# Kernel optimization log

Hardware: AMD Instinct MI355X
Metric: run time of the kernel (lower is better)

The kernel has to match this reference:

```python
import jax, jax.numpy as jnp
import numpy as np

N = 50000
NUM_GRAPHS = 64
EPS = 1e-16  # PyG softmax denominator epsilon


def _gat_conv(x, src, dst, W, a_src, a_dst, b, heads, out_ch):
    n = x.shape[0]
    h = (x @ W).reshape(n, heads, out_ch)                    # [N,H,C]
    al_s = jnp.einsum('nhc,hc->nh', h, a_src)                # [N,H]
    al_d = jnp.einsum('nhc,hc->nh', h, a_dst)                # [N,H]
    e = jax.nn.leaky_relu(al_s[src] + al_d[dst], 0.2)        # [E,H]
    emax = jax.ops.segment_max(e, dst, num_segments=n)       # [N,H]
    ee = jnp.exp(e - emax[dst])
    den = jax.ops.segment_sum(ee, dst, num_segments=n)       # [N,H]
    alpha = ee / (den[dst] + EPS)                            # [E,H]
    msg = h[src] * alpha[:, :, None]                         # [E,H,C]
    out = jax.ops.segment_sum(msg, dst, num_segments=n)      # [N,H,C]
    return out.reshape(n, heads * out_ch) + b


def setup_inputs() -> dict:
    key = jax.random.key(0)
    ks = jax.random.split(key, 16)
    E = 250000
    x = jax.random.normal(ks[0], (N, 11), dtype=jnp.float32)
    edge_index = jax.random.randint(ks[1], (2, E), 0, N, dtype=jnp.int64)
    batch = jnp.sort(jax.random.randint(ks[2], (N,), 0, NUM_GRAPHS, dtype=jnp.int64))
    def glorot(k, shape):
        fan = shape[0] + shape[-1]
        return jax.random.uniform(k, shape, jnp.float32, -1.0, 1.0) * np.sqrt(6.0 / fan)
    return {
        'x': x, 'edge_index': edge_index, 'batch': batch,
        'W1': glorot(ks[3], (11, 8 * 128)),
        'a1s': glorot(ks[4], (8, 128)), 'a1d': glorot(ks[5], (8, 128)),
        'b1': jnp.zeros((8 * 128,), jnp.float32),
        'W2': glorot(ks[6], (1024, 8 * 64)),
        'a2s': glorot(ks[7], (8, 64)), 'a2d': glorot(ks[8], (8, 64)),
        'b2': jnp.zeros((8 * 64,), jnp.float32),
        'W3': glorot(ks[9], (512, 4 * 32)),
        'a3s': glorot(ks[10], (4, 32)), 'a3d': glorot(ks[11], (4, 32)),
        'b3': jnp.zeros((4 * 32,), jnp.float32),
        'Wout': glorot(ks[12], (128, 1)),
        'bout': jnp.zeros((1,), jnp.float32),
    }


def reference(x, edge_index, batch, W1, a1s, a1d, b1, W2, a2s, a2d, b2,
              W3, a3s, a3d, b3, Wout, bout):
    n = x.shape[0]
    # GATConv adds self-loops by default
    loop = jnp.arange(n, dtype=edge_index.dtype)
    src = jnp.concatenate([edge_index[0], loop])
    dst = jnp.concatenate([edge_index[1], loop])
    h = jax.nn.leaky_relu(_gat_conv(x, src, dst, W1, a1s, a1d, b1, 8, 128), 0.01)
    h = jax.nn.leaky_relu(_gat_conv(h, src, dst, W2, a2s, a2d, b2, 8, 64), 0.01)
    h = jax.nn.leaky_relu(_gat_conv(h, src, dst, W3, a3s, a3d, b3, 4, 32), 0.01)
    # global mean pool over graphs
    sums = jax.ops.segment_sum(h, batch, num_segments=NUM_GRAPHS)      # [G,128]
    cnt = jax.ops.segment_sum(jnp.ones((n,), h.dtype), batch, num_segments=NUM_GRAPHS)
    pooled = sums / jnp.maximum(cnt, 1.0)[:, None]
    return pooled @ Wout + bout                                        # [G,1]
```

## Files before the change

kernel.cpp:

```cpp
#include <hip/hip_runtime.h>

#define EPS 1e-16f

typedef __attribute__((ext_vector_type(8))) short short8;
typedef __attribute__((ext_vector_type(4))) float f32x4;

__device__ __forceinline__ float b2f(unsigned short u) {
    return __uint_as_float(((unsigned)u) << 16);
}
__device__ __forceinline__ unsigned short f2b(float f) {
    unsigned u = __float_as_uint(f);
    u += 0x7fffu + ((u >> 16) & 1u);
    return (unsigned short)(u >> 16);
}

typedef __attribute__((address_space(3))) void lds_vp;
typedef __attribute__((address_space(1))) const void glb_vp;
__device__ __forceinline__ void load_lds16(const unsigned short* g,
                                           unsigned short* l) {
    __builtin_amdgcn_global_load_lds((glb_vp*)g, (lds_vp*)l, 16, 0, 0);
}

__global__ void init_deg_kernel(int* deg, int N) {
    int i = blockIdx.x * blockDim.x + threadIdx.x;
    if (i < N) deg[i] = 1;
}

__global__ void hist_kernel(const int* __restrict__ ei, int E, int N, int* deg) {
    int e = blockIdx.x * blockDim.x + threadIdx.x;
    if (e < E) {
        int d = ei[E + e];
        if ((unsigned)d < (unsigned)N) atomicAdd(&deg[d], 1);
    }
}

__global__ void scan_block_kernel(const int* __restrict__ deg,
                                  int* __restrict__ rowst,
                                  int* __restrict__ bsum, int N) {
    __shared__ int s[256];
    int t = threadIdx.x, b = blockIdx.x;
    int i = b * 256 + t;
    s[t] = (i < N) ? deg[i] : 0;
    __syncthreads();
    for (int o = 1; o < 256; o <<= 1) {
        int a = (t >= o) ? s[t - o] : 0;
        __syncthreads();
        s[t] += a;
        __syncthreads();
    }
    if (i < N) rowst[i + 1] = s[t];
    if (t == 255) bsum[b] = s[255];
}

__global__ void scan_top_kernel(const int* __restrict__ bsum,
                                int* __restrict__ boff, int NB) {
    __shared__ int psum[65];
    int t = threadIdx.x;
    int chunk = (NB + 63) / 64;
    int lo = t * chunk, hi = lo + chunk;
    if (lo > NB) lo = NB;
    if (hi > NB) hi = NB;
    int s = 0;
    for (int i = lo; i < hi; i++) s += bsum[i];
    psum[t + 1] = s;
    __syncthreads();
    if (t == 0) {
        psum[0] = 0;
        for (int i = 1; i <= 64; i++) psum[i] += psum[i - 1];
    }
    __syncthreads();
    int run = psum[t];
    for (int i = lo; i < hi; i++) {
        boff[i] = run;
        run += bsum[i];
    }
}

__global__ void scan_finish_kernel(int* __restrict__ rowst,
                                   const int* __restrict__ boff,
                                   const int* __restrict__ deg,
                                   int* __restrict__ srcs,
                                   int* __restrict__ cursor, int N) {
    int i = blockIdx.x * 256 + threadIdx.x;
    if (i == 0) rowst[0] = 0;
    if (i < N) {
        int incl = rowst[i + 1] + boff[blockIdx.x];
        rowst[i + 1] = incl;
        int st = incl - deg[i];
        srcs[st] = i;
        cursor[i] = st + 1;
    }
}

__global__ void scatter_kernel(const int* __restrict__ ei, int E, int N,
                               int* cursor, int* srcs) {
    int e = blockIdx.x * blockDim.x + threadIdx.x;
    if (e < E) {
        int d = ei[E + e];
        if ((unsigned)d < (unsigned)N) {
            int p = atomicAdd(&cursor[d], 1);
            int s = ei[e];
            if ((unsigned)s >= (unsigned)N) s = d;
            srcs[p] = s;
        }
    }
}

__global__ void wprep_kernel(const float* __restrict__ W1,
                             const float* __restrict__ W2,
                             const float* __restrict__ W3,
                             unsigned short* __restrict__ wt2,
                             unsigned short* __restrict__ wt3,
                             unsigned short* __restrict__ w1sk) {
    int i = blockIdx.x * blockDim.x + threadIdx.x;
    if (i < 1024 * 512) {
        int k = i / 512, n = i % 512;
        wt2[(size_t)n * 1024 + k] = f2b(W2[i]);
    } else if (i < 1024 * 512 + 512 * 128) {
        int j = i - 1024 * 512;
        int k = j / 128, n = j % 128;
        wt3[(size_t)n * 512 + k] = f2b(W3[j]);
    } else if (i < 1024 * 512 + 512 * 128 + 8 * 128 * 32) {
        int q = i - (1024 * 512 + 512 * 128);
        int h = q >> 12, rem = q & 4095;
        int c = rem >> 5, kk = rem & 31;
        int off = (h == 7) ? 16 : 0;
        float v = 0.f;
        int k = kk - off;
        if (k >= 0 && k < 11) v = W1[k * 1024 + h * 128 + c];
        w1sk[q] = f2b(v);
    }
}

__global__ void wa1_kernel(const float* __restrict__ W1,
                           const float* __restrict__ a1s,
                           const float* __restrict__ a1d,
                           float* __restrict__ w_as, float* __restrict__ w_ad) {
    int t = threadIdx.x;
    if (t >= 88) return;
    int h = t / 11, k = t % 11;
    float s = 0.f, d = 0.f;
    for (int c = 0; c < 128; c++) {
        float w = W1[k * 1024 + h * 128 + c];
        s += w * a1s[h * 128 + c];
        d += w * a1d[h * 128 + c];
    }
    w_as[h * 16 + k] = s;
    w_ad[h * 16 + k] = d;
}

__global__ void al1_kernel(const float* __restrict__ x,
                           const float* __restrict__ w_as,
                           const float* __restrict__ w_ad,
                           float* __restrict__ als, float* __restrict__ ald,
                           int N) {
    int i = blockIdx.x * blockDim.x + threadIdx.x;
    if (i >= N * 8) return;
    int n = i >> 3, h = i & 7;
    float s = 0.f, d = 0.f;
#pragma unroll
    for (int k = 0; k < 11; k++) {
        float xv = x[n * 11 + k];
        s += xv * w_as[h * 16 + k];
        d += xv * w_ad[h * 16 + k];
    }
    als[i] = s;
    ald[i] = d;
}

template <int H>
__global__ void mden_kernel(const float* __restrict__ als,
                            const float* __restrict__ ald,
                            const int* __restrict__ rowst,
                            const int* __restrict__ srcs,
                            float* __restrict__ escr, int N) {
    int i = blockIdx.x * blockDim.x + threadIdx.x;
    if (i >= N * H) return;
    int n = i / H, h = i % H;
    float aldn = ald[i];
    int start = rowst[n], end = rowst[n + 1];
    const int CH = 4;
    float m = -1e30f;
    for (int idx = start; idx < end; idx += CH) {
        int mc = end - idx;
        if (mc > CH) mc = CH;
        int ss[CH];
        float lv[CH];
#pragma unroll
        for (int j = 0; j < CH; j++)
            if (j < mc) ss[j] = srcs[idx + j];
#pragma unroll
        for (int j = 0; j < CH; j++)
            if (j < mc) lv[j] = als[ss[j] * H + h];
#pragma unroll
        for (int j = 0; j < CH; j++)
            if (j < mc) {
                float v = lv[j] + aldn;
                v = v > 0.f ? v : 0.2f * v;
                escr[(size_t)(idx + j) * H + h] = v;
                m = fmaxf(m, v);
            }
    }
    float den = 0.f;
    for (int idx = start; idx < end; idx += CH) {
        int mc = end - idx;
        if (mc > CH) mc = CH;
        float lv[CH];
#pragma unroll
        for (int j = 0; j < CH; j++)
            if (j < mc) lv[j] = escr[(size_t)(idx + j) * H + h];
#pragma unroll
        for (int j = 0; j < CH; j++)
            if (j < mc) den += expf(lv[j] - m);
    }
    float dinv = 1.0f / (den + EPS);
    for (int idx = start; idx < end; idx += CH) {
        int mc = end - idx;
        if (mc > CH) mc = CH;
        float lv[CH];
#pragma unroll
        for (int j = 0; j < CH; j++)
            if (j < mc) lv[j] = escr[(size_t)(idx + j) * H + h];
#pragma unroll
        for (int j = 0; j < CH; j++)
            if (j < mc)
                escr[(size_t)(idx + j) * H + h] = expf(lv[j] - m) * dinv;
    }
}

__global__ void aggx_kernel(const float* __restrict__ x,
                            const float* __restrict__ escr,
                            const int* __restrict__ rowst,
                            const int* __restrict__ srcs,
                            unsigned short* __restrict__ A2, int N) {
    int n = blockIdx.x;
    int t = threadIdx.x;
    int h = t >> 4, k = t & 15;
    int start = rowst[n], end = rowst[n + 1];
    float acc = 0.f;
    const int CH = 4;
    for (int idx = start; idx < end; idx += CH) {
        int mc = end - idx;
        if (mc > CH) mc = CH;
        int ss[CH];
        float av[CH], xv[CH];
#pragma unroll
        for (int j = 0; j < CH; j++)
            if (j < mc) ss[j] = srcs[idx + j];
#pragma unroll
        for (int j = 0; j < CH; j++)
            if (j < mc) av[j] = escr[(size_t)(idx + j) * 8 + h];
#pragma unroll
        for (int j = 0; j < CH; j++)
            if (j < mc) xv[j] = (k < 11) ? x[ss[j] * 11 + k] : 0.f;
#pragma unroll
        for (int j = 0; j < CH; j++)
            if (j < mc) acc += av[j] * xv[j];
    }
    A2[(size_t)n * 128 + t] = f2b(acc);
}

template <bool EPI, int HB, int CC, bool SK>
__global__ __launch_bounds__(256) void gemm_mfma(
    const unsigned short* __restrict__ A, const unsigned short* __restrict__ Bt,
    unsigned short* __restrict__ C, const float* __restrict__ bias,
    const float* __restrict__ a_s, const float* __restrict__ a_d,
    float* __restrict__ als, float* __restrict__ ald, int H, int M, int N,
    int K, int lda) {
    int NX = gridDim.x;
    int bid = blockIdx.y * NX + blockIdx.x;
    int win = bid & (8 * NX - 1);
    int mg = bid / (8 * NX);
    int m_t = mg * 8 + (win & 7);
    int n_t = win >> 3;
    int bm = m_t * 128, bn = n_t * 128;
    if (bm >= M) return;

    union SMem {
        struct {
            unsigned short As[2][128 * 32];
            unsigned short Bs[2][128 * 32];
        } k;
        unsigned short Ct[128 * 132];
    };
    __shared__ __align__(16) SMem sm;
    auto& As = sm.k.As;
    auto& Bs = sm.k.Bs;
    auto& Ct = sm.Ct;

    int t = threadIdx.x;
    int w = t >> 6, lane = t & 63;
    int quad = lane >> 4, l16 = lane & 15;
    int wr = (w >> 1) * 64, wc = (w & 1) * 64;

    int kofs = 0;
    const unsigned short* Bb = Bt;
    if (SK) {
        kofs = n_t * 16;
        if (kofs > lda - 32) kofs = lda - 32;
        Bb = Bt + (size_t)n_t * 128 * 32;
    }

    int c0 = w * 128 + lane;
    int c1 = c0 + 64;
    int r0 = c0 >> 2, p0 = c0 & 3;
    int r1 = c1 >> 2, p1 = c1 & 3;
    int j0 = (p0 - (r0 >> 1)) & 3;
    int j1 = (p1 - (r1 >> 1)) & 3;
    int ga0 = bm + r0;
    if (ga0 >= M) ga0 = M - 1;
    int ga1 = bm + r1;
    if (ga1 >= M) ga1 = M - 1;
    const unsigned short* Ag0 = A + (size_t)ga0 * lda + kofs + j0 * 8;
    const unsigned short* Ag1 = A + (size_t)ga1 * lda + kofs + j1 * 8;
    size_t br0 = SK ? (size_t)r0 : (size_t)(bn + r0);
    size_t br1 = SK ? (size_t)r1 : (size_t)(bn + r1);
    const unsigned short* Bg0 = Bb + br0 * K + j0 * 8;
    const unsigned short* Bg1 = Bb + br1 * K + j1 * 8;

    auto stage = [&](int st, int k0) {
        load_lds16(Ag0 + k0, &As[st][(w * 128) * 8]);
        load_lds16(Ag1 + k0, &As[st][(w * 128 + 64) * 8]);
        load_lds16(Bg0 + k0, &Bs[st][(w * 128) * 8]);
        load_lds16(Bg1 + k0, &Bs[st][(w * 128 + 64) * 8]);
    };

    int aoff[4], boff4[4];
#pragma unroll
    for (int i = 0; i < 4; i++) {
        int ra = wr + i * 16 + l16;
        aoff[i] = ra * 32 + (((quad + (ra >> 1)) & 3) * 8);
        int rb = wc + i * 16 + l16;
        boff4[i] = rb * 32 + (((quad + (rb >> 1)) & 3) * 8);
    }

    f32x4 acc[4][4] = {};
    stage(0, 0);
    int st = 0;
    for (int k0 = 0; k0 < K; k0 += 32, st ^= 1) {
        __syncthreads();
        if (k0 + 32 < K) stage(st ^ 1, k0 + 32);
        short8 a[4], b[4];
#pragma unroll
        for (int mi = 0; mi < 4; mi++) a[mi] = *(const short8*)&As[st][aoff[mi]];
#pragma unroll
        for (int ni = 0; ni < 4; ni++) b[ni] = *(const short8*)&Bs[st][boff4[ni]];
#pragma unroll
        for (int mi = 0; mi < 4; mi++)
#pragma unroll
            for (int ni = 0; ni < 4; ni++)
                acc[mi][ni] = __builtin_amdgcn_mfma_f32_16x16x32_bf16(
                    a[mi], b[ni], acc[mi][ni], 0, 0, 0);
    }
    __syncthreads();

#pragma unroll
    for (int mi = 0; mi < 4; mi++) {
#pragma unroll
        for (int r = 0; r < 4; r++) {
            int rl = wr + mi * 16 + quad * 4 + r;
#pragma unroll
            for (int ni = 0; ni < 4; ni++) {
                int cl = wc + ni * 16 + l16;
                float v = acc[mi][ni][r];
                if (EPI) {
                    v += bias[bn + cl];
                    v = v > 0.f ? v : 0.01f * v;
                }
                Ct[rl * 132 + cl] = f2b(v);
            }
        }
    }
    __syncthreads();
#pragma unroll
    for (int p = 0; p < 16; p++) {
        int q = p * 256 + t;
        int row = q >> 5, c8 = q & 31;
        if (bm + row < M) {
            uint2 v = *(const uint2*)&Ct[row * 132 + c8 * 4];
            *(uint2*)&C[(size_t)(bm + row) * N + bn + c8 * 4] = v;
        }
    }
    if (HB > 0) {
        for (int pi = t; pi < 128 * HB; pi += 256) {
            int row = pi / HB, hl = pi % HB;
            if (bm + row >= M) continue;
            int hg = bn / CC + hl;
            const unsigned short* rp = &Ct[row * 132 + hl * CC];
            const float* asp = a_s + hg * CC;
            const float* adp = a_d + hg * CC;
            float s = 0.f, d = 0.f;
#pragma unroll
            for (int c = 0; c < CC; c++) {
                float v = b2f(rp[c]);
                s += v * asp[c];
                d += v * adp[c];
            }
            als[(size_t)(bm + row) * H + hg] = s;
            ald[(size_t)(bm + row) * H + hg] = d;
        }
    }
}

template <int H, int C>
__global__ void agg_fused4(const unsigned short* __restrict__ hin,
                           const float* __restrict__ als,
                           const float* __restrict__ ald,
                           const int* __restrict__ rowst,
                           const int* __restrict__ srcs,
                           const float* __restrict__ bias,
                           unsigned short* __restrict__ out, int N) {
    constexpr int HC = H * C;
    constexpr int TPH = C / 4;
    int n = blockIdx.x;
    int t = threadIdx.x;
    int c = t * 4;
    int hh = c / C;
    int li = (c % C) / 4;
    int start = rowst[n], end = rowst[n + 1];
    float aldn = ald[n * H + hh];
    float m = -1e30f;
    for (int idx = start + li; idx < end; idx += TPH) {
        float v = als[srcs[idx] * H + hh] + aldn;
        v = v > 0.f ? v : 0.2f * v;
        m = fmaxf(m, v);
    }
#pragma unroll
    for (int o = 1; o < TPH; o <<= 1) m = fmaxf(m, __shfl_xor(m, o));
    float den = 0.f;
    for (int idx = start + li; idx < end; idx += TPH) {
        float v = als[srcs[idx] * H + hh] + aldn;
        v = v > 0.f ? v : 0.2f * v;
        den += expf(v - m);
    }
#pragma unroll
    for (int o = 1; o < TPH; o <<= 1) den += __shfl_xor(den, o);
    float dinv = 1.0f / (den + EPS);

    float a0 = 0.f, a1 = 0.f, a2 = 0.f, a3 = 0.f;
    const int CH = 4;
    for (int idx = start; idx < end; idx += CH) {
        int mc = end - idx;
        if (mc > CH) mc = CH;
        int ss[CH];
        float lv[CH];
        ushort4 uv[CH];
#pragma unroll
        for (int j = 0; j < CH; j++)
            if (j < mc) ss[j] = srcs[idx + j];
#pragma unroll
        for (int j = 0; j < CH; j++)
            if (j < mc) lv[j] = als[ss[j] * H + hh];
#pragma unroll
        for (int j = 0; j < CH; j++)
            if (j < mc) uv[j] = *(const ushort4*)(hin + (size_t)ss[j] * HC + c);
#pragma unroll
        for (int j = 0; j < CH; j++)
            if (j < mc) {
                float v = lv[j] + aldn;
                v = v > 0.f ? v : 0.2f * v;
                float a = expf(v - m) * dinv;
                a0 += a * b2f(uv[j].x);
                a1 += a * b2f(uv[j].y);
                a2 += a * b2f(uv[j].z);
                a3 += a * b2f(uv[j].w);
            }
    }
    float v0 = a0 + bias[c], v1 = a1 + bias[c + 1];
    float v2 = a2 + bias[c + 2], v3 = a3 + bias[c + 3];
    ushort4 o;
    o.x = f2b(v0 > 0.f ? v0 : 0.01f * v0);
    o.y = f2b(v1 > 0.f ? v1 : 0.01f * v1);
    o.z = f2b(v2 > 0.f ? v2 : 0.01f * v2);
    o.w = f2b(v3 > 0.f ? v3 : 0.01f * v3);
    *(ushort4*)&out[(size_t)n * HC + c] = o;
}

template <int H, int C>
__global__ void agg_fused2(const unsigned short* __restrict__ hin,
                           const float* __restrict__ als,
                           const float* __restrict__ ald,
                           const int* __restrict__ rowst,
                           const int* __restrict__ srcs,
                           const float* __restrict__ bias,
                           unsigned short* __restrict__ out, int N) {
    constexpr int HC = H * C;
    constexpr int TPH = C / 2;
    int n = blockIdx.x;
    int t = threadIdx.x;
    int c = t * 2;
    int hh = c / C;
    int li = (c % C) / 2;
    int start = rowst[n], end = rowst[n + 1];
    float aldn = ald[n * H + hh];
    float m = -1e30f;
    for (int idx = start + li; idx < end; idx += TPH) {
        float v = als[srcs[idx] * H + hh] + aldn;
        v = v > 0.f ? v : 0.2f * v;
        m = fmaxf(m, v);
    }
#pragma unroll
    for (int o = 1; o < TPH; o <<= 1) m = fmaxf(m, __shfl_xor(m, o));
    float den = 0.f;
    for (int idx = start + li; idx < end; idx += TPH) {
        float v = als[srcs[idx] * H + hh] + aldn;
        v = v > 0.f ? v : 0.2f * v;
        den += expf(v - m);
    }
#pragma unroll
    for (int o = 1; o < TPH; o <<= 1) den += __shfl_xor(den, o);
    float dinv = 1.0f / (den + EPS);

    float a0 = 0.f, a1 = 0.f;
    const int CH = 4;
    for (int idx = start; idx < end; idx += CH) {
        int mc = end - idx;
        if (mc > CH) mc = CH;
        int ss[CH];
        float lv[CH];
        ushort2 uv[CH];
#pragma unroll
        for (int j = 0; j < CH; j++)
            if (j < mc) ss[j] = srcs[idx + j];
#pragma unroll
        for (int j = 0; j < CH; j++)
            if (j < mc) lv[j] = als[ss[j] * H + hh];
#pragma unroll
        for (int j = 0; j < CH; j++)
            if (j < mc) uv[j] = *(const ushort2*)(hin + (size_t)ss[j] * HC + c);
#pragma unroll
        for (int j = 0; j < CH; j++)
            if (j < mc) {
                float v = lv[j] + aldn;
                v = v > 0.f ? v : 0.2f * v;
                float a = expf(v - m) * dinv;
                a0 += a * b2f(uv[j].x);
                a1 += a * b2f(uv[j].y);
            }
    }
    float v0 = a0 + bias[c], v1 = a1 + bias[c + 1];
    ushort2 o;
    o.x = f2b(v0 > 0.f ? v0 : 0.01f * v0);
    o.y = f2b(v1 > 0.f ? v1 : 0.01f * v1);
    *(ushort2*)&out[(size_t)n * HC + c] = o;
}

__global__ void pool_init_kernel(float* pool, int GC) {
    int i = blockIdx.x * blockDim.x + threadIdx.x;
    if (i < GC) pool[i] = 0.f;
}

__global__ void pool_partial_kernel(const unsigned short* __restrict__ h3,
                                    const int* __restrict__ batch,
                                    float* __restrict__ pool, int N, int G) {
    int lo = blockIdx.x * 128;
    int hi = lo + 128;
    if (hi > N) hi = N;
    if (lo >= N) return;
    int t = threadIdx.x;
    int cur = batch[lo];
    float acc = 0.f;
    for (int n = lo; n < hi; n++) {
        int g = batch[n];
        if (g != cur) {
            if ((unsigned)cur < (unsigned)G) atomicAdd(&pool[cur * 128 + t], acc);
            acc = 0.f;
            cur = g;
        }
        acc += b2f(h3[(size_t)n * 128 + t]);
    }
    if ((unsigned)cur < (unsigned)G) atomicAdd(&pool[cur * 128 + t], acc);
}

__global__ void head_kernel(const float* __restrict__ pool,
                            const int* __restrict__ batch,
                            const float* __restrict__ Wout,
                            const float* __restrict__ bout,
                            float* __restrict__ out, int N) {
    int g = blockIdx.x;
    int t = threadIdx.x;
    int lo, hi;
    {
        int a = 0, b = N;
        while (a < b) { int mid = (a + b) >> 1; if (batch[mid] < g) a = mid + 1; else b = mid; }
        lo = a;
        a = lo; b = N;
        while (a < b) { int mid = (a + b) >> 1; if (batch[mid] < g + 1) a = mid + 1; else b = mid; }
        hi = a;
    }
    float c = (float)(hi - lo);
    c = c > 1.f ? c : 1.f;
    float v = (pool[g * 128 + t] / c) * Wout[t];
    for (int o = 32; o; o >>= 1) v += __shfl_xor(v, o);
    __shared__ float partial[2];
    if ((t & 63) == 0) partial[t >> 6] = v;
    __syncthreads();
    if (t == 0) out[g] = partial[0] + partial[1] + bout[0];
}

extern "C" void kernel_launch(void* const* d_in, const int* in_sizes, int n_in,
                              void* d_out, int out_size, void* d_ws,
                              size_t ws_size, hipStream_t stream) {
    const float* x = (const float*)d_in[0];
    const int* ei = (const int*)d_in[1];
    const int* batch = (const int*)d_in[2];
    const float* W1 = (const float*)d_in[3];
    const float* a1s = (const float*)d_in[4];
    const float* a1d = (const float*)d_in[5];
    const float* b1 = (const float*)d_in[6];
    const float* W2 = (const float*)d_in[7];
    const float* a2s = (const float*)d_in[8];
    const float* a2d = (const float*)d_in[9];
    const float* b2 = (const float*)d_in[10];
    const float* W3 = (const float*)d_in[11];
    const float* a3s = (const float*)d_in[12];
    const float* a3d = (const float*)d_in[13];
    const float* b3 = (const float*)d_in[14];
    const float* Wout = (const float*)d_in[15];
    const float* bout = (const float*)d_in[16];
    float* out = (float*)d_out;

    const int N = in_sizes[0] / 11;
    const int E = in_sizes[1] / 2;
    const int Etot = E + N;
    const int G = out_size;
    const int NB = (N + 255) / 256;
    const int MT = ((N + 127) / 128 + 7) / 8 * 8;

    char* ws = (char*)d_ws;
    size_t off = 0;
    auto alloc = [&](size_t bytes) -> void* {
        void* p = ws + off;
        off += (bytes + 255) & ~(size_t)255;
        return p;
    };
    unsigned short* buf1 = (unsigned short*)alloc((size_t)N * 1024 * 2);
    unsigned short* buf2 = (unsigned short*)alloc((size_t)N * 1024 * 2);
    float* als = (float*)alloc((size_t)N * 8 * 4);
    float* ald = (float*)alloc((size_t)N * 8 * 4);
    float* escr = (float*)alloc((size_t)Etot * 8 * 4);
    int* rowst = (int*)alloc((size_t)(N + 1) * 4);
    int* cursor = (int*)alloc((size_t)N * 4);
    int* srcs = (int*)alloc((size_t)Etot * 4);
    int* deg = (int*)alloc((size_t)N * 4);
    int* bsum = (int*)alloc((size_t)NB * 4);
    int* boff = (int*)alloc((size_t)NB * 4);
    float* pool = (float*)alloc((size_t)G * 128 * 4);
    unsigned short* aggx = (unsigned short*)alloc((size_t)N * 128 * 2);
    unsigned short* w1sk = (unsigned short*)alloc((size_t)8 * 128 * 32 * 2);
    unsigned short* wt2 = (unsigned short*)alloc((size_t)1024 * 512 * 2);
    unsigned short* wt3 = (unsigned short*)alloc((size_t)512 * 128 * 2);
    float* w_as = (float*)alloc(8 * 16 * 4);
    float* w_ad = (float*)alloc(8 * 16 * 4);

    int nb = (N + 255) / 256;
    int eb = (E + 255) / 256;

    init_deg_kernel<<<nb, 256, 0, stream>>>(deg, N);
    hist_kernel<<<eb, 256, 0, stream>>>(ei, E, N, deg);
    scan_block_kernel<<<NB, 256, 0, stream>>>(deg, rowst, bsum, N);
    scan_top_kernel<<<1, 64, 0, stream>>>(bsum, boff, NB);
    scan_finish_kernel<<<NB, 256, 0, stream>>>(rowst, boff, deg, srcs, cursor,
                                               N);
    scatter_kernel<<<eb, 256, 0, stream>>>(ei, E, N, cursor, srcs);

    const int WTOT = 1024 * 512 + 512 * 128 + 8 * 128 * 32;
    wprep_kernel<<<(WTOT + 255) / 256, 256, 0, stream>>>(W1, W2, W3, wt2, wt3,
                                                         w1sk);
    wa1_kernel<<<1, 128, 0, stream>>>(W1, a1s, a1d, w_as, w_ad);

    al1_kernel<<<(N * 8 + 255) / 256, 256, 0, stream>>>(x, w_as, w_ad, als, ald,
                                                        N);
    mden_kernel<8><<<(N * 8 + 255) / 256, 256, 0, stream>>>(als, ald, rowst,
                                                            srcs, escr, N);
    aggx_kernel<<<N, 128, 0, stream>>>(x, escr, rowst, srcs, aggx, N);
    gemm_mfma<true, 0, 1, true><<<dim3(8, MT), 256, 0, stream>>>(
        aggx, w1sk, buf2, b1, nullptr, nullptr, nullptr, nullptr, 0, N, 1024,
        32, 128);

    gemm_mfma<false, 2, 64, false><<<dim3(4, MT), 256, 0, stream>>>(
        buf2, wt2, buf1, nullptr, a2s, a2d, als, ald, 8, N, 512, 1024, 1024);
    agg_fused4<8, 64><<<N, 128, 0, stream>>>(buf1, als, ald, rowst, srcs, b2,
                                             buf2, N);

    gemm_mfma<false, 4, 32, false><<<dim3(1, MT), 256, 0, stream>>>(
        buf2, wt3, buf1, nullptr, a3s, a3d, als, ald, 4, N, 128, 512, 512);
    agg_fused2<4, 32><<<N, 64, 0, stream>>>(buf1, als, ald, rowst, srcs, b3,
                                            buf2, N);

    pool_init_kernel<<<(G * 128 + 255) / 256, 256, 0, stream>>>(pool, G * 128);
    pool_partial_kernel<<<(N + 127) / 128, 128, 0, stream>>>(buf2, batch, pool,
                                                             N, G);
    head_kernel<<<G, 128, 0, stream>>>(pool, batch, Wout, bout, out, N);
}
```

Measured before the change: 482.3 us.

## Add double-buffered async-LDS MFMA GEMM with swizzle and tile raster for layers 2-3

Adds a new gemm_pipe kernel that stages A and B tiles into LDS through global_load_lds with a two-deep buffer, so the next K-tile loads while MFMAs run on the current one. It uses an XOR-swizzled LDS layout, groups blocks into 8-row M windows for L2 reuse, and shares LDS between the staging buffers and the output tile through a union. Layers 2 and 3 now call it in place of gemm_mfma. In exchange it adds hand-placed waitcnt and barriers that depend on exact vmcnt accounting, and uses more LDS per block.

```diff
diff --git a/kernel.cpp b/kernel.cpp
--- a/kernel.cpp
+++ b/kernel.cpp
@@ -387,6 +387,144 @@
             if (bm + row >= M) continue;
             int hg = bn / CC + hl;
             const unsigned short* rp = &Ct[row * 132 + hl * CC];
+            const float* asp = a_s + hg * CC;
+            const float* adp = a_d + hg * CC;
+            float s = 0.f, d = 0.f;
+#pragma unroll
+            for (int c = 0; c < CC; c++) {
+                float v = b2f(rp[c]);
+                s += v * asp[c];
+                d += v * adp[c];
+            }
+            als[(size_t)(bm + row) * H + hg] = s;
+            ald[(size_t)(bm + row) * H + hg] = d;
+        }
+    }
+}
+
+template <int HB, int CC>
+__global__ __launch_bounds__(256, 2) void gemm_pipe(
+    const unsigned short* __restrict__ A, const unsigned short* __restrict__ Bt,
+    unsigned short* __restrict__ C, const float* __restrict__ a_s,
+    const float* __restrict__ a_d, float* __restrict__ als,
+    float* __restrict__ ald, int H, int M, int N, int K) {
+    int NX = gridDim.x;
+    int bid = blockIdx.y * NX + blockIdx.x;
+    int win = bid & (8 * NX - 1);
+    int mg = bid / (8 * NX);
+    int m_t = mg * 8 + (win & 7);
+    int n_t = win >> 3;
+    int bm = m_t * 128, bn = n_t * 128;
+    if (bm >= M) return;
+
+    union SMem {
+        struct {
+            unsigned short As[2][128 * 64];
+            unsigned short Bs[2][128 * 64];
+        } k;
+        unsigned short Ct[128 * 132];
+    };
+    __shared__ __align__(16) SMem sm;
+
+    int t = threadIdx.x;
+    int w = t >> 6, lane = t & 63;
+    int quad = lane >> 4, l16 = lane & 15;
+    int wr = (w >> 1) * 64, wc = (w & 1) * 64;
+
+    int srow = lane >> 3;
+    int gsl = (lane & 7) ^ srow;
+    const unsigned short* Ag[4];
+    const unsigned short* Bg[4];
+#pragma unroll
+    for (int j = 0; j < 4; j++) {
+        int row = (j * 4 + w) * 8 + srow;
+        int ga = bm + row;
+        if (ga > M - 1) ga = M - 1;
+        Ag[j] = A + (size_t)ga * K + gsl * 8;
+        Bg[j] = Bt + (size_t)(bn + row) * K + gsl * 8;
+    }
+    auto stage = [&](int st, int kt) {
+        int ko = kt * 64;
+#pragma unroll
+        for (int j = 0; j < 4; j++) {
+            load_lds16(Ag[j] + ko, &sm.k.As[st][(j * 4 + w) * 512]);
+            load_lds16(Bg[j] + ko, &sm.k.Bs[st][(j * 4 + w) * 512]);
+        }
+    };
+
+    int arow[4], brow[4];
+#pragma unroll
+    for (int i = 0; i < 4; i++) {
+        arow[i] = (wr + i * 16 + l16) * 64;
+        brow[i] = (wc + i * 16 + l16) * 64;
+    }
+    int sw = l16 & 7;
+
+    f32x4 acc[4][4] = {};
+    int NT = K >> 6;
+    stage(0, 0);
+    if (NT > 1) stage(1, 1);
+    for (int tt = 0; tt < NT; tt++) {
+        int bb = tt & 1;
+        if (tt + 1 < NT)
+            asm volatile("s_waitcnt vmcnt(8)" ::: "memory");
+        else
+            asm volatile("s_waitcnt vmcnt(0)" ::: "memory");
+        __builtin_amdgcn_s_barrier();
+        __builtin_amdgcn_sched_barrier(0);
+#pragma unroll
+        for (int ks = 0; ks < 2; ks++) {
+            short8 a[4], b[4];
+            int so = ((ks * 4 + quad) ^ sw) * 8;
+#pragma unroll
+            for (int mi = 0; mi < 4; mi++)
+                a[mi] = *(const short8*)&sm.k.As[bb][arow[mi] + so];
+#pragma unroll
+            for (int ni = 0; ni < 4; ni++)
+                b[ni] = *(const short8*)&sm.k.Bs[bb][brow[ni] + so];
+            __builtin_amdgcn_s_setprio(1);
+#pragma unroll
+            for (int mi = 0; mi < 4; mi++)
+#pragma unroll
+                for (int ni = 0; ni < 4; ni++)
+                    acc[mi][ni] = __builtin_amdgcn_mfma_f32_16x16x32_bf16(
+                        a[mi], b[ni], acc[mi][ni], 0, 0, 0);
+            __builtin_amdgcn_s_setprio(0);
+        }
+        asm volatile("s_waitcnt lgkmcnt(0)" ::: "memory");
+        __builtin_amdgcn_s_barrier();
+        if (tt + 2 < NT) stage(bb, tt + 2);
+    }
+    __syncthreads();
+
+#pragma unroll
+    for (int mi = 0; mi < 4; mi++) {
+#pragma unroll
+        for (int r = 0; r < 4; r++) {
+            int rl = wr + mi * 16 + quad * 4 + r;
+#pragma unroll
+            for (int ni = 0; ni < 4; ni++) {
+                int cl = wc + ni * 16 + l16;
+                sm.Ct[rl * 132 + cl] = f2b(acc[mi][ni][r]);
+            }
+        }
+    }
+    __syncthreads();
+#pragma unroll
+    for (int p = 0; p < 16; p++) {
+        int q = p * 256 + t;
+        int row = q >> 5, c8 = q & 31;
+        if (bm + row < M) {
+            uint2 v = *(const uint2*)&sm.Ct[row * 132 + c8 * 4];
+            *(uint2*)&C[(size_t)(bm + row) * N + bn + c8 * 4] = v;
+        }
+    }
+    if (HB > 0) {
+        for (int pi = t; pi < 128 * HB; pi += 256) {
+            int row = pi / HB, hl = pi % HB;
+            if (bm + row >= M) continue;
+            int hg = bn / CC + hl;
+            const unsigned short* rp = &sm.Ct[row * 132 + hl * CC];
             const float* asp = a_s + hg * CC;
             const float* adp = a_d + hg * CC;
             float s = 0.f, d = 0.f;
@@ -678,13 +816,13 @@
         aggx, w1sk, buf2, b1, nullptr, nullptr, nullptr, nullptr, 0, N, 1024,
         32, 128);
 
-    gemm_mfma<false, 2, 64, false><<<dim3(4, MT), 256, 0, stream>>>(
-        buf2, wt2, buf1, nullptr, a2s, a2d, als, ald, 8, N, 512, 1024, 1024);
+    gemm_pipe<2, 64><<<dim3(4, MT), 256, 0, stream>>>(
+        buf2, wt2, buf1, a2s, a2d, als, ald, 8, N, 512, 1024);
     agg_fused4<8, 64><<<N, 128, 0, stream>>>(buf1, als, ald, rowst, srcs, b2,
                                              buf2, N);
 
-    gemm_mfma<false, 4, 32, false><<<dim3(1, MT), 256, 0, stream>>>(
-        buf2, wt3, buf1, nullptr, a3s, a3d, als, ald, 4, N, 128, 512, 512);
+    gemm_pipe<4, 32><<<dim3(1, MT), 256, 0, stream>>>(
+        buf2, wt3, buf1, a3s, a3d, als, ald, 4, N, 128, 512);
     agg_fused2<4, 32><<<N, 64, 0, stream>>>(buf1, als, ald, rowst, srcs, b3,
                                             buf2, N);
 
```

Measured after the change: 472.8 us. -2.0%, faster.
